# Optimization experiments

Hardware: AMD Instinct MI355X
Metric: run time of the kernel (lower is better)

## Reference

```python
import jax, jax.numpy as jnp
import numpy as np

D_MODEL = 1024
N_HEADS = 16


def setup_inputs() -> dict:
    key = jax.random.key(0)
    k1, k2, k3 = jax.random.split(key, 3)
    B, S = 2, 2048
    std_qkv = (2.0 / (D_MODEL + 3 * D_MODEL)) ** 0.5
    std_out = (2.0 / (D_MODEL + D_MODEL)) ** 0.5
    X = jax.random.normal(k1, (B, S, D_MODEL), dtype=jnp.float32)
    W_qkv = jax.random.normal(k2, (3 * D_MODEL, D_MODEL), dtype=jnp.float32) * std_qkv
    W_out = jax.random.normal(k3, (D_MODEL, D_MODEL), dtype=jnp.float32) * std_out
    return {"X": X, "W_qkv": W_qkv, "W_out": W_out}


def reference(X, W_qkv, W_out):
    B, S, D = X.shape
    H = N_HEADS
    dk = D // H
    # qkv projection: (..., d) @ W^T -> (..., 3d)
    qkv = jnp.einsum('bsd,ed->bse', X, W_qkv)
    Q, K, V = jnp.split(qkv, 3, axis=-1)
    # split heads: (B, S, H*dk) -> (B, H, S, dk)
    def heads(t):
        return t.reshape(B, S, H, dk).transpose(0, 2, 1, 3)
    Q, K, V = heads(Q), heads(K), heads(V)
    # scaled scores (B, H, S, S)
    scores = jnp.einsum('bhqd,bhkd->bhqk', Q, K) / jnp.sqrt(jnp.float32(dk))
    causal = jnp.tril(jnp.ones((S, S), dtype=bool))
    scores = jnp.where(causal, scores.astype(jnp.float32), -jnp.inf)
    weights = jax.nn.softmax(scores, axis=-1).astype(X.dtype)
    out = jnp.einsum('bhqk,bhkd->bhqd', weights, V)
    out = out.transpose(0, 2, 1, 3).reshape(B, S, D)
    return jnp.einsum('bsd,od->bso', out, W_out)
```

## Files before the change

### kernel.cpp

```cpp
#include <hip/hip_runtime.h>

typedef __bf16 bf16;
typedef __bf16 bf16x4v __attribute__((ext_vector_type(4)));
typedef __bf16 bf16x8 __attribute__((ext_vector_type(8)));
typedef float f32x4 __attribute__((ext_vector_type(4)));

#define MFMA16(a, b, c) __builtin_amdgcn_mfma_f32_16x16x32_bf16((a), (b), (c), 0, 0, 0)

#define SEQ 2048
#define DM 1024
#define NH 16

__global__ __launch_bounds__(256) void cvt_bf16(const float* __restrict__ s,
                                                bf16* __restrict__ d, int n4) {
    const int i = blockIdx.x * 256 + threadIdx.x;
    if (i < n4) {
        const float4 v = ((const float4*)s)[i];
        bf16x4v o;
        o.x = (bf16)v.x; o.y = (bf16)v.y; o.z = (bf16)v.z; o.w = (bf16)v.w;
        ((bf16x4v*)d)[i] = o;
    }
}

template <typename CT>
__global__ __launch_bounds__(256) void gemm_nt(const bf16* __restrict__ A,
                                               const bf16* __restrict__ B,
                                               CT* __restrict__ C,
                                               int M, int N, int K) {
    __shared__ bf16 As[128 * 40];
    __shared__ bf16 Bs[128 * 40];

    const int tid = threadIdx.x;
    const int lane = tid & 63, w = tid >> 6;
    const int quad = lane >> 4, l15 = lane & 15;
    const int wm = (w & 1) * 64, wn = (w >> 1) * 64;
    const int rowBase = blockIdx.y * 128, colBase = blockIdx.x * 128;
    const int srow = tid >> 2, sseg = tid & 3;

    f32x4 acc[4][4] = {};

    for (int k0 = 0; k0 < K; k0 += 32) {
        __syncthreads();
#pragma unroll
        for (int r = 0; r < 2; ++r) {
            const int row = srow + r * 64;
            *(bf16x8*)(As + row * 40 + sseg * 8) =
                *(const bf16x8*)(A + (size_t)(rowBase + row) * K + k0 + sseg * 8);
            *(bf16x8*)(Bs + row * 40 + sseg * 8) =
                *(const bf16x8*)(B + (size_t)(colBase + row) * K + k0 + sseg * 8);
        }
        __syncthreads();

        bf16x8 af[4], bfr[4];
#pragma unroll
        for (int i = 0; i < 4; ++i) {
            af[i]  = *(const bf16x8*)(As + (wm + i * 16 + l15) * 40 + quad * 8);
            bfr[i] = *(const bf16x8*)(Bs + (wn + i * 16 + l15) * 40 + quad * 8);
        }
#pragma unroll
        for (int i = 0; i < 4; ++i)
#pragma unroll
            for (int j = 0; j < 4; ++j)
                acc[i][j] = MFMA16(af[i], bfr[j], acc[i][j]);
    }

#pragma unroll
    for (int i = 0; i < 4; ++i)
#pragma unroll
        for (int j = 0; j < 4; ++j)
#pragma unroll
            for (int r = 0; r < 4; ++r)
                C[(size_t)(rowBase + wm + i * 16 + quad * 4 + r) * N +
                  colBase + wn + j * 16 + l15] = (CT)acc[i][j][r];
}

__global__ __launch_bounds__(256) void gemm_qkv(const bf16* __restrict__ A,
                                                const bf16* __restrict__ B,
                                                bf16* __restrict__ qkbuf,
                                                bf16* __restrict__ vtg) {
    __shared__ bf16 As[128 * 40];
    __shared__ bf16 Bs[128 * 40];

    const int K = DM, tid = threadIdx.x;
    const int lane = tid & 63, w = tid >> 6;
    const int quad = lane >> 4, l15 = lane & 15;
    const int wm = (w & 1) * 64, wn = (w >> 1) * 64;
    const int rowBase = blockIdx.y * 128, colBase = blockIdx.x * 128;
    const int srow = tid >> 2, sseg = tid & 3;

    f32x4 acc[4][4] = {};

    for (int k0 = 0; k0 < K; k0 += 32) {
        __syncthreads();
#pragma unroll
        for (int r = 0; r < 2; ++r) {
            const int row = srow + r * 64;
            *(bf16x8*)(As + row * 40 + sseg * 8) =
                *(const bf16x8*)(A + (size_t)(rowBase + row) * K + k0 + sseg * 8);
            *(bf16x8*)(Bs + row * 40 + sseg * 8) =
                *(const bf16x8*)(B + (size_t)(colBase + row) * K + k0 + sseg * 8);
        }
        __syncthreads();

        bf16x8 af[4], bfr[4];
#pragma unroll
        for (int i = 0; i < 4; ++i) {
            af[i]  = *(const bf16x8*)(As + (wm + i * 16 + l15) * 40 + quad * 8);
            bfr[i] = *(const bf16x8*)(Bs + (wn + i * 16 + l15) * 40 + quad * 8);
        }
#pragma unroll
        for (int i = 0; i < 4; ++i)
#pragma unroll
            for (int j = 0; j < 4; ++j)
                acc[i][j] = MFMA16(af[i], bfr[j], acc[i][j]);
    }

    if (colBase < 2 * DM) {
#pragma unroll
        for (int i = 0; i < 4; ++i)
#pragma unroll
            for (int j = 0; j < 4; ++j)
#pragma unroll
                for (int r = 0; r < 4; ++r)
                    qkbuf[(size_t)(rowBase + wm + i * 16 + quad * 4 + r) * 2048 +
                          colBase + wn + j * 16 + l15] = (bf16)acc[i][j][r];
    } else {
#pragma unroll
        for (int i = 0; i < 4; ++i) {
            const int row0 = rowBase + wm + i * 16 + quad * 4;
            const int b = row0 >> 11, s = row0 & 2047;
#pragma unroll
            for (int j = 0; j < 4; ++j) {
                const int col = colBase + wn + j * 16 + l15 - 2 * DM;
                bf16x4v pk;
#pragma unroll
                for (int r = 0; r < 4; ++r) pk[r] = (bf16)acc[i][j][r];
                *(bf16x4v*)(vtg + (size_t)(b * DM + col) * SEQ + s) = pk;
            }
        }
    }
}

__global__ __launch_bounds__(256) void attn_fwd(const bf16* __restrict__ qk,
                                                const bf16* __restrict__ vtg,
                                                bf16* __restrict__ ao) {
    __shared__ bf16 Ks[64 * 72];
    __shared__ bf16 Vts[64 * 72];
    __shared__ bf16 Pt[4][16 * 72];

    const int tid = threadIdx.x;
    const int lane = tid & 63, w = tid >> 6;
    const int quad = lane >> 4, l15 = lane & 15;
    const int bh = blockIdx.x;
    const int qtile = 31 - blockIdx.y;
    const int b = bh >> 4, h = bh & 15;
    const int qbase = qtile * 64;
    const int wq = qbase + w * 16;

    const bf16* qkb = qk + (size_t)b * SEQ * 2048;
    const bf16* vb  = vtg + (size_t)bh * 64 * SEQ;

    bf16x8 q_lo, q_hi;
    {
        const bf16* qp = qkb + (size_t)(wq + l15) * 2048 + h * 64 + quad * 8;
        bf16x8 lo = *(const bf16x8*)qp;
        bf16x8 hi = *(const bf16x8*)(qp + 32);
#pragma unroll
        for (int i = 0; i < 8; ++i) {
            q_lo[i] = (bf16)((float)lo[i] * 0.125f);
            q_hi[i] = (bf16)((float)hi[i] * 0.125f);
        }
    }

    f32x4 o[4] = {};
    float mi = -1e30f, li = 0.f;

    const int kr0 = tid >> 3;
    const int ksg = tid & 7;

    const int nkt = qtile + 1;
    for (int kt = 0; kt < nkt; ++kt) {
        const int k0 = kt * 64;
        __syncthreads();
#pragma unroll
        for (int half = 0; half < 2; ++half) {
            const int kr = kr0 + half * 32;
            *(bf16x8*)(Ks + kr * 72 + ksg * 8) =
                *(const bf16x8*)(qkb + (size_t)(k0 + kr) * 2048 + DM + h * 64 + ksg * 8);
            *(bf16x8*)(Vts + kr * 72 + ksg * 8) =
                *(const bf16x8*)(vb + (size_t)kr * SEQ + k0 + ksg * 8);
        }
        __syncthreads();

        if (k0 <= wq + 15) {
            f32x4 s[4];
#pragma unroll
            for (int t = 0; t < 4; ++t) {
                const bf16* kp = Ks + (t * 16 + l15) * 72 + quad * 8;
                bf16x8 k_lo = *(const bf16x8*)kp;
                bf16x8 k_hi = *(const bf16x8*)(kp + 32);
                f32x4 z = {};
                z = MFMA16(k_lo, q_lo, z);
                z = MFMA16(k_hi, q_hi, z);
                s[t] = z;
            }
            const int qg = wq + l15;
            if (k0 + 63 > wq) {
#pragma unroll
                for (int t = 0; t < 4; ++t)
#pragma unroll
                    for (int r = 0; r < 4; ++r)
                        if (k0 + t * 16 + quad * 4 + r > qg) s[t][r] = -1e30f;
            }
            float mx = s[0][0];
#pragma unroll
            for (int t = 0; t < 4; ++t)
#pragma unroll
                for (int r = 0; r < 4; ++r) mx = fmaxf(mx, s[t][r]);
            mx = fmaxf(mx, __shfl_xor(mx, 16));
            mx = fmaxf(mx, __shfl_xor(mx, 32));
            const float mnew = fmaxf(mi, mx);
            const float alpha = __expf(mi - mnew);
            mi = mnew;

            float rsum = 0.f;
            bf16x4v pb[4];
#pragma unroll
            for (int t = 0; t < 4; ++t)
#pragma unroll
                for (int r = 0; r < 4; ++r) {
                    float p = __expf(s[t][r] - mnew);
                    rsum += p;
                    pb[t][r] = (bf16)p;
                }
            rsum += __shfl_xor(rsum, 16);
            rsum += __shfl_xor(rsum, 32);
            li = li * alpha + rsum;
#pragma unroll
            for (int dt = 0; dt < 4; ++dt)
#pragma unroll
                for (int r = 0; r < 4; ++r) o[dt][r] *= alpha;

            bf16* P = &Pt[w][0];
#pragma unroll
            for (int t = 0; t < 4; ++t)
                *(bf16x4v*)(P + l15 * 72 + t * 16 + quad * 4) = pb[t];
            asm volatile("s_waitcnt lgkmcnt(0)" ::: "memory");

            bf16x8 pf0 = *(const bf16x8*)(P + l15 * 72 + quad * 8);
            bf16x8 pf1 = *(const bf16x8*)(P + l15 * 72 + 32 + quad * 8);
#pragma unroll
            for (int dt = 0; dt < 4; ++dt) {
                const bf16* vp = Vts + (dt * 16 + l15) * 72 + quad * 8;
                bf16x8 v0 = *(const bf16x8*)vp;
                bf16x8 v1 = *(const bf16x8*)(vp + 32);
                o[dt] = MFMA16(v0, pf0, o[dt]);
                o[dt] = MFMA16(v1, pf1, o[dt]);
            }
        }
    }

    const float inv = 1.f / li;
    bf16* aop = ao + (size_t)(b * SEQ + wq + l15) * DM + h * 64;
#pragma unroll
    for (int dt = 0; dt < 4; ++dt) {
        bf16x4v ov;
#pragma unroll
        for (int r = 0; r < 4; ++r) ov[r] = (bf16)(o[dt][r] * inv);
        *(bf16x4v*)(aop + dt * 16 + quad * 4) = ov;
    }
}

extern "C" void kernel_launch(void* const* d_in, const int* in_sizes, int n_in,
                              void* d_out, int out_size, void* d_ws, size_t ws_size,
                              hipStream_t stream) {
    const float* X    = (const float*)d_in[0];
    const float* Wqkv = (const float*)d_in[1];
    const float* Wout = (const float*)d_in[2];
    float* out = (float*)d_out;

    const int M = 2 * SEQ;
    const size_t nX    = (size_t)M * DM;
    const size_t nWqkv = (size_t)3 * DM * DM;
    const size_t nWout = (size_t)DM * DM;
    const size_t nQK   = (size_t)M * 2 * DM;
    const size_t nVT   = (size_t)2 * DM * SEQ;
    const size_t nAO   = (size_t)M * DM;

    if (ws_size < (nX + nWqkv + nWout + nQK + nVT + nAO) * sizeof(bf16)) return;

    bf16* Xb    = (bf16*)d_ws;
    bf16* Wqkvb = Xb + nX;
    bf16* Woutb = Wqkvb + nWqkv;
    bf16* qkbuf = Woutb + nWout;
    bf16* vtg   = qkbuf + nQK;
    bf16* ao    = vtg + nVT;

    cvt_bf16<<<dim3((int)(nX / 4 / 256)),    256, 0, stream>>>(X,    Xb,    (int)(nX / 4));
    cvt_bf16<<<dim3((int)(nWqkv / 4 / 256)), 256, 0, stream>>>(Wqkv, Wqkvb, (int)(nWqkv / 4));
    cvt_bf16<<<dim3((int)(nWout / 4 / 256)), 256, 0, stream>>>(Wout, Woutb, (int)(nWout / 4));

    gemm_qkv<<<dim3(3 * DM / 128, M / 128), 256, 0, stream>>>(Xb, Wqkvb, qkbuf, vtg);
    attn_fwd<<<dim3(2 * NH, SEQ / 64), 256, 0, stream>>>(qkbuf, vtg, ao);
    gemm_nt<float><<<dim3(DM / 128, M / 128), 256, 0, stream>>>(ao, Woutb, out, M, DM, DM);
}
```

Measured before the change: 194.4 us.

## Fuse conversions, stage V transpose via LDS, use 128-key tiles with register prefetch

```diff
diff --git a/kernel.cpp b/kernel.cpp
--- a/kernel.cpp
+++ b/kernel.cpp
@@ -11,15 +11,23 @@
 #define DM 1024
 #define NH 16
 
-__global__ __launch_bounds__(256) void cvt_bf16(const float* __restrict__ s,
-                                                bf16* __restrict__ d, int n4) {
+__global__ __launch_bounds__(256) void cvt_all(const float* __restrict__ X,
+                                               const float* __restrict__ Wq,
+                                               const float* __restrict__ Wo,
+                                               bf16* __restrict__ Xb,
+                                               bf16* __restrict__ Wqb,
+                                               bf16* __restrict__ Wob) {
     const int i = blockIdx.x * 256 + threadIdx.x;
-    if (i < n4) {
-        const float4 v = ((const float4*)s)[i];
-        bf16x4v o;
-        o.x = (bf16)v.x; o.y = (bf16)v.y; o.z = (bf16)v.z; o.w = (bf16)v.w;
-        ((bf16x4v*)d)[i] = o;
-    }
+    const int N1 = (4 * 1024 * 1024) / 4;
+    const int N2 = (3 * 1024 * 1024) / 4;
+    const float* s; bf16* d; int off;
+    if (i < N1)            { s = X;  d = Xb;  off = i; }
+    else if (i < N1 + N2)  { s = Wq; d = Wqb; off = i - N1; }
+    else                   { s = Wo; d = Wob; off = i - N1 - N2; }
+    const float4 v = ((const float4*)s)[off];
+    bf16x4v o;
+    o.x = (bf16)v.x; o.y = (bf16)v.y; o.z = (bf16)v.z; o.w = (bf16)v.w;
+    ((bf16x4v*)d)[off] = o;
 }
 
 template <typename CT>
@@ -78,8 +86,9 @@
                                                 const bf16* __restrict__ B,
                                                 bf16* __restrict__ qkbuf,
                                                 bf16* __restrict__ vtg) {
-    __shared__ bf16 As[128 * 40];
-    __shared__ bf16 Bs[128 * 40];
+    __shared__ bf16 smem[10240];
+    bf16* As = smem;
+    bf16* Bs = smem + 5120;
 
     const int K = DM, tid = threadIdx.x;
     const int lane = tid & 63, w = tid >> 6;
@@ -125,17 +134,32 @@
                     qkbuf[(size_t)(rowBase + wm + i * 16 + quad * 4 + r) * 2048 +
                           colBase + wn + j * 16 + l15] = (bf16)acc[i][j][r];
     } else {
-#pragma unroll
-        for (int i = 0; i < 4; ++i) {
-            const int row0 = rowBase + wm + i * 16 + quad * 4;
-            const int b = row0 >> 11, s = row0 & 2047;
-#pragma unroll
-            for (int j = 0; j < 4; ++j) {
-                const int col = colBase + wn + j * 16 + l15 - 2 * DM;
-                bf16x4v pk;
-#pragma unroll
-                for (int r = 0; r < 4; ++r) pk[r] = (bf16)acc[i][j][r];
-                *(bf16x4v*)(vtg + (size_t)(b * DM + col) * SEQ + s) = pk;
+        bf16* T = smem;
+        const int vcolBase = colBase - 2 * DM;
+        const int bb = rowBase >> 11;
+        const int sBase = rowBase & 2047;
+        const int drow0 = tid >> 4, seg = tid & 15;
+#pragma unroll
+        for (int c = 0; c < 2; ++c) {
+            __syncthreads();
+            if ((w >> 1) == c) {
+#pragma unroll
+                for (int i = 0; i < 4; ++i)
+#pragma unroll
+                    for (int j = 0; j < 4; ++j) {
+                        bf16x4v pk;
+#pragma unroll
+                        for (int r = 0; r < 4; ++r) pk[r] = (bf16)acc[i][j][r];
+                        *(bf16x4v*)(T + (j * 16 + l15) * 136 + wm + i * 16 + quad * 4) = pk;
+                    }
+            }
+            __syncthreads();
+#pragma unroll
+            for (int rr = 0; rr < 4; ++rr) {
+                const int drow = rr * 16 + drow0;
+                *(bf16x8*)(vtg + (size_t)(bb * DM + vcolBase + c * 64 + drow) * SEQ +
+                           sBase + seg * 8) =
+                    *(const bf16x8*)(T + drow * 136 + seg * 8);
             }
         }
     }
@@ -144,9 +168,9 @@
 __global__ __launch_bounds__(256) void attn_fwd(const bf16* __restrict__ qk,
                                                 const bf16* __restrict__ vtg,
                                                 bf16* __restrict__ ao) {
-    __shared__ bf16 Ks[64 * 72];
-    __shared__ bf16 Vts[64 * 72];
-    __shared__ bf16 Pt[4][16 * 72];
+    __shared__ bf16 Ks[128 * 72];
+    __shared__ bf16 Vts[64 * 136];
+    __shared__ bf16 Pt[4][16 * 136];
 
     const int tid = threadIdx.x;
     const int lane = tid & 63, w = tid >> 6;
@@ -175,87 +199,100 @@
     f32x4 o[4] = {};
     float mi = -1e30f, li = 0.f;
 
-    const int kr0 = tid >> 3;
-    const int ksg = tid & 7;
-
-    const int nkt = qtile + 1;
+    bf16x8 pk[4], pv[4];
+    const int nkt = (qbase >> 7) + 1;
+
+    {
+        const int k0 = 0;
+#pragma unroll
+        for (int i = 0; i < 4; ++i) {
+            const int slot = tid + i * 256;
+            pk[i] = *(const bf16x8*)(qkb + (size_t)(k0 + (slot >> 3)) * 2048 + DM + h * 64 + (slot & 7) * 8);
+            pv[i] = *(const bf16x8*)(vb + (size_t)(slot >> 4) * SEQ + k0 + (slot & 15) * 8);
+        }
+    }
+
     for (int kt = 0; kt < nkt; ++kt) {
-        const int k0 = kt * 64;
-        __syncthreads();
-#pragma unroll
-        for (int half = 0; half < 2; ++half) {
-            const int kr = kr0 + half * 32;
-            *(bf16x8*)(Ks + kr * 72 + ksg * 8) =
-                *(const bf16x8*)(qkb + (size_t)(k0 + kr) * 2048 + DM + h * 64 + ksg * 8);
-            *(bf16x8*)(Vts + kr * 72 + ksg * 8) =
-                *(const bf16x8*)(vb + (size_t)kr * SEQ + k0 + ksg * 8);
-        }
-        __syncthreads();
-
-        if (k0 <= wq + 15) {
-            f32x4 s[4];
-#pragma unroll
-            for (int t = 0; t < 4; ++t) {
-                const bf16* kp = Ks + (t * 16 + l15) * 72 + quad * 8;
-                bf16x8 k_lo = *(const bf16x8*)kp;
-                bf16x8 k_hi = *(const bf16x8*)(kp + 32);
-                f32x4 z = {};
-                z = MFMA16(k_lo, q_lo, z);
-                z = MFMA16(k_hi, q_hi, z);
-                s[t] = z;
-            }
-            const int qg = wq + l15;
-            if (k0 + 63 > wq) {
-#pragma unroll
-                for (int t = 0; t < 4; ++t)
-#pragma unroll
-                    for (int r = 0; r < 4; ++r)
-                        if (k0 + t * 16 + quad * 4 + r > qg) s[t][r] = -1e30f;
-            }
-            float mx = s[0][0];
-#pragma unroll
-            for (int t = 0; t < 4; ++t)
-#pragma unroll
-                for (int r = 0; r < 4; ++r) mx = fmaxf(mx, s[t][r]);
-            mx = fmaxf(mx, __shfl_xor(mx, 16));
-            mx = fmaxf(mx, __shfl_xor(mx, 32));
-            const float mnew = fmaxf(mi, mx);
-            const float alpha = __expf(mi - mnew);
-            mi = mnew;
-
-            float rsum = 0.f;
-            bf16x4v pb[4];
-#pragma unroll
-            for (int t = 0; t < 4; ++t)
-#pragma unroll
-                for (int r = 0; r < 4; ++r) {
-                    float p = __expf(s[t][r] - mnew);
-                    rsum += p;
-                    pb[t][r] = (bf16)p;
-                }
-            rsum += __shfl_xor(rsum, 16);
-            rsum += __shfl_xor(rsum, 32);
-            li = li * alpha + rsum;
-#pragma unroll
-            for (int dt = 0; dt < 4; ++dt)
-#pragma unroll
-                for (int r = 0; r < 4; ++r) o[dt][r] *= alpha;
-
-            bf16* P = &Pt[w][0];
-#pragma unroll
-            for (int t = 0; t < 4; ++t)
-                *(bf16x4v*)(P + l15 * 72 + t * 16 + quad * 4) = pb[t];
-            asm volatile("s_waitcnt lgkmcnt(0)" ::: "memory");
-
-            bf16x8 pf0 = *(const bf16x8*)(P + l15 * 72 + quad * 8);
-            bf16x8 pf1 = *(const bf16x8*)(P + l15 * 72 + 32 + quad * 8);
+        const int k0 = kt * 128;
+        __syncthreads();
+#pragma unroll
+        for (int i = 0; i < 4; ++i) {
+            const int slot = tid + i * 256;
+            *(bf16x8*)(Ks + (slot >> 3) * 72 + (slot & 7) * 8) = pk[i];
+            *(bf16x8*)(Vts + (slot >> 4) * 136 + (slot & 15) * 8) = pv[i];
+        }
+        __syncthreads();
+        if (kt + 1 < nkt) {
+            const int kn = k0 + 128;
+#pragma unroll
+            for (int i = 0; i < 4; ++i) {
+                const int slot = tid + i * 256;
+                pk[i] = *(const bf16x8*)(qkb + (size_t)(kn + (slot >> 3)) * 2048 + DM + h * 64 + (slot & 7) * 8);
+                pv[i] = *(const bf16x8*)(vb + (size_t)(slot >> 4) * SEQ + kn + (slot & 15) * 8);
+            }
+        }
+
+        const int t_used = min(8, ((wq + 15 - k0) >> 4) + 1);
+        f32x4 s[8];
+        for (int t = 0; t < t_used; ++t) {
+            const bf16* kp = Ks + (t * 16 + l15) * 72 + quad * 8;
+            bf16x8 k_lo = *(const bf16x8*)kp;
+            bf16x8 k_hi = *(const bf16x8*)(kp + 32);
+            f32x4 z = {};
+            z = MFMA16(k_lo, q_lo, z);
+            z = MFMA16(k_hi, q_hi, z);
+            s[t] = z;
+        }
+        const int qg = wq + l15;
+        if (k0 + 127 > wq) {
+            for (int t = 0; t < t_used; ++t)
+#pragma unroll
+                for (int r = 0; r < 4; ++r)
+                    if (k0 + t * 16 + quad * 4 + r > qg) s[t][r] = -1e30f;
+        }
+        float mx = -1e30f;
+        for (int t = 0; t < t_used; ++t)
+#pragma unroll
+            for (int r = 0; r < 4; ++r) mx = fmaxf(mx, s[t][r]);
+        mx = fmaxf(mx, __shfl_xor(mx, 16));
+        mx = fmaxf(mx, __shfl_xor(mx, 32));
+        const float mnew = fmaxf(mi, mx);
+        const float alpha = __expf(mi - mnew);
+        mi = mnew;
+
+        bf16* P = &Pt[w][0];
+        float rsum = 0.f;
+        for (int t = 0; t < t_used; ++t) {
+            bf16x4v pb;
+#pragma unroll
+            for (int r = 0; r < 4; ++r) {
+                float p = __expf(s[t][r] - mnew);
+                rsum += p;
+                pb[r] = (bf16)p;
+            }
+            *(bf16x4v*)(P + l15 * 136 + t * 16 + quad * 4) = pb;
+        }
+        if (t_used & 1) {
+            bf16x4v z4 = {};
+            *(bf16x4v*)(P + l15 * 136 + t_used * 16 + quad * 4) = z4;
+        }
+        rsum += __shfl_xor(rsum, 16);
+        rsum += __shfl_xor(rsum, 32);
+        li = li * alpha + rsum;
+#pragma unroll
+        for (int dt = 0; dt < 4; ++dt)
+#pragma unroll
+            for (int r = 0; r < 4; ++r) o[dt][r] *= alpha;
+
+        asm volatile("s_waitcnt lgkmcnt(0)" ::: "memory");
+
+        const int f_used = (t_used + 1) >> 1;
+        for (int f = 0; f < f_used; ++f) {
+            bf16x8 pf = *(const bf16x8*)(P + l15 * 136 + f * 32 + quad * 8);
 #pragma unroll
             for (int dt = 0; dt < 4; ++dt) {
-                const bf16* vp = Vts + (dt * 16 + l15) * 72 + quad * 8;
-                bf16x8 v0 = *(const bf16x8*)vp;
-                bf16x8 v1 = *(const bf16x8*)(vp + 32);
-                o[dt] = MFMA16(v0, pf0, o[dt]);
-                o[dt] = MFMA16(v1, pf1, o[dt]);
+                bf16x8 vf = *(const bf16x8*)(Vts + (dt * 16 + l15) * 136 + f * 32 + quad * 8);
+                o[dt] = MFMA16(vf, pf, o[dt]);
             }
         }
     }
@@ -296,9 +333,8 @@
     bf16* vtg   = qkbuf + nQK;
     bf16* ao    = vtg + nVT;
 
-    cvt_bf16<<<dim3((int)(nX / 4 / 256)),    256, 0, stream>>>(X,    Xb,    (int)(nX / 4));
-    cvt_bf16<<<dim3((int)(nWqkv / 4 / 256)), 256, 0, stream>>>(Wqkv, Wqkvb, (int)(nWqkv / 4));
-    cvt_bf16<<<dim3((int)(nWout / 4 / 256)), 256, 0, stream>>>(Wout, Woutb, (int)(nWout / 4));
+    const int nCvt4 = (int)((nX + nWqkv + nWout) / 4);
+    cvt_all<<<dim3(nCvt4 / 256), 256, 0, stream>>>(X, Wqkv, Wout, Xb, Wqkvb, Woutb);
 
     gemm_qkv<<<dim3(3 * DM / 128, M / 128), 256, 0, stream>>>(Xb, Wqkvb, qkbuf, vtg);
     attn_fwd<<<dim3(2 * NH, SEQ / 64), 256, 0, stream>>>(qkbuf, vtg, ao);
```

Measured after the change: 230.3 us. 18.4% more time.

## Fuse conversions, use direct global-to-LDS loads, widen attention q-tiles, retile out GEMM

Applied to the files above, without the earlier changes.

```diff
diff --git a/kernel.cpp b/kernel.cpp
--- a/kernel.cpp
+++ b/kernel.cpp
@@ -11,102 +11,64 @@
 #define DM 1024
 #define NH 16
 
-__global__ __launch_bounds__(256) void cvt_bf16(const float* __restrict__ s,
-                                                bf16* __restrict__ d, int n4) {
+typedef __attribute__((address_space(3))) unsigned int lds_u32;
+typedef __attribute__((address_space(1))) const unsigned int glb_u32;
+
+__device__ __forceinline__ void gld16(const bf16* g, bf16* l) {
+    __builtin_amdgcn_global_load_lds((glb_u32*)g, (lds_u32*)l, 16, 0, 0);
+}
+
+__global__ __launch_bounds__(256) void cvt_all(const float* __restrict__ X,
+                                               const float* __restrict__ Wq,
+                                               const float* __restrict__ Wo,
+                                               bf16* __restrict__ Xb,
+                                               bf16* __restrict__ Wqb,
+                                               bf16* __restrict__ Wob) {
     const int i = blockIdx.x * 256 + threadIdx.x;
-    if (i < n4) {
-        const float4 v = ((const float4*)s)[i];
-        bf16x4v o;
-        o.x = (bf16)v.x; o.y = (bf16)v.y; o.z = (bf16)v.z; o.w = (bf16)v.w;
-        ((bf16x4v*)d)[i] = o;
-    }
-}
-
-template <typename CT>
-__global__ __launch_bounds__(256) void gemm_nt(const bf16* __restrict__ A,
-                                               const bf16* __restrict__ B,
-                                               CT* __restrict__ C,
-                                               int M, int N, int K) {
-    __shared__ bf16 As[128 * 40];
-    __shared__ bf16 Bs[128 * 40];
-
-    const int tid = threadIdx.x;
-    const int lane = tid & 63, w = tid >> 6;
-    const int quad = lane >> 4, l15 = lane & 15;
-    const int wm = (w & 1) * 64, wn = (w >> 1) * 64;
-    const int rowBase = blockIdx.y * 128, colBase = blockIdx.x * 128;
-    const int srow = tid >> 2, sseg = tid & 3;
-
-    f32x4 acc[4][4] = {};
-
-    for (int k0 = 0; k0 < K; k0 += 32) {
-        __syncthreads();
-#pragma unroll
-        for (int r = 0; r < 2; ++r) {
-            const int row = srow + r * 64;
-            *(bf16x8*)(As + row * 40 + sseg * 8) =
-                *(const bf16x8*)(A + (size_t)(rowBase + row) * K + k0 + sseg * 8);
-            *(bf16x8*)(Bs + row * 40 + sseg * 8) =
-                *(const bf16x8*)(B + (size_t)(colBase + row) * K + k0 + sseg * 8);
-        }
-        __syncthreads();
-
-        bf16x8 af[4], bfr[4];
-#pragma unroll
-        for (int i = 0; i < 4; ++i) {
-            af[i]  = *(const bf16x8*)(As + (wm + i * 16 + l15) * 40 + quad * 8);
-            bfr[i] = *(const bf16x8*)(Bs + (wn + i * 16 + l15) * 40 + quad * 8);
-        }
-#pragma unroll
-        for (int i = 0; i < 4; ++i)
-#pragma unroll
-            for (int j = 0; j < 4; ++j)
-                acc[i][j] = MFMA16(af[i], bfr[j], acc[i][j]);
-    }
-
-#pragma unroll
-    for (int i = 0; i < 4; ++i)
-#pragma unroll
-        for (int j = 0; j < 4; ++j)
-#pragma unroll
-            for (int r = 0; r < 4; ++r)
-                C[(size_t)(rowBase + wm + i * 16 + quad * 4 + r) * N +
-                  colBase + wn + j * 16 + l15] = (CT)acc[i][j][r];
+    const int N1 = (4 * 1024 * 1024) / 4;
+    const int N2 = (3 * 1024 * 1024) / 4;
+    const float* s; bf16* d; int off;
+    if (i < N1)            { s = X;  d = Xb;  off = i; }
+    else if (i < N1 + N2)  { s = Wq; d = Wqb; off = i - N1; }
+    else                   { s = Wo; d = Wob; off = i - N1 - N2; }
+    const float4 v = ((const float4*)s)[off];
+    bf16x4v o;
+    o.x = (bf16)v.x; o.y = (bf16)v.y; o.z = (bf16)v.z; o.w = (bf16)v.w;
+    ((bf16x4v*)d)[off] = o;
 }
 
 __global__ __launch_bounds__(256) void gemm_qkv(const bf16* __restrict__ A,
                                                 const bf16* __restrict__ B,
                                                 bf16* __restrict__ qkbuf,
                                                 bf16* __restrict__ vtg) {
-    __shared__ bf16 As[128 * 40];
-    __shared__ bf16 Bs[128 * 40];
+    __shared__ bf16 As[128 * 32];
+    __shared__ bf16 Bs[128 * 32];
 
     const int K = DM, tid = threadIdx.x;
     const int lane = tid & 63, w = tid >> 6;
     const int quad = lane >> 4, l15 = lane & 15;
     const int wm = (w & 1) * 64, wn = (w >> 1) * 64;
     const int rowBase = blockIdx.y * 128, colBase = blockIdx.x * 128;
-    const int srow = tid >> 2, sseg = tid & 3;
 
     f32x4 acc[4][4] = {};
 
     for (int k0 = 0; k0 < K; k0 += 32) {
         __syncthreads();
 #pragma unroll
-        for (int r = 0; r < 2; ++r) {
-            const int row = srow + r * 64;
-            *(bf16x8*)(As + row * 40 + sseg * 8) =
-                *(const bf16x8*)(A + (size_t)(rowBase + row) * K + k0 + sseg * 8);
-            *(bf16x8*)(Bs + row * 40 + sseg * 8) =
-                *(const bf16x8*)(B + (size_t)(colBase + row) * K + k0 + sseg * 8);
+        for (int i = 0; i < 2; ++i) {
+            const int c = w * 64 + i * 256 + lane;
+            gld16(A + (size_t)(rowBase + (c >> 2)) * K + k0 + (c & 3) * 8,
+                  As + (w * 64 + i * 256) * 8);
+            gld16(B + (size_t)(colBase + (c >> 2)) * K + k0 + (c & 3) * 8,
+                  Bs + (w * 64 + i * 256) * 8);
         }
         __syncthreads();
 
         bf16x8 af[4], bfr[4];
 #pragma unroll
         for (int i = 0; i < 4; ++i) {
-            af[i]  = *(const bf16x8*)(As + (wm + i * 16 + l15) * 40 + quad * 8);
-            bfr[i] = *(const bf16x8*)(Bs + (wn + i * 16 + l15) * 40 + quad * 8);
+            af[i]  = *(const bf16x8*)(As + (wm + i * 16 + l15) * 32 + quad * 8);
+            bfr[i] = *(const bf16x8*)(Bs + (wn + i * 16 + l15) * 32 + quad * 8);
         }
 #pragma unroll
         for (int i = 0; i < 4; ++i)
@@ -128,17 +90,70 @@
 #pragma unroll
         for (int i = 0; i < 4; ++i) {
             const int row0 = rowBase + wm + i * 16 + quad * 4;
-            const int b = row0 >> 11, s = row0 & 2047;
+            const int bb = row0 >> 11, s = row0 & 2047;
 #pragma unroll
             for (int j = 0; j < 4; ++j) {
                 const int col = colBase + wn + j * 16 + l15 - 2 * DM;
                 bf16x4v pk;
 #pragma unroll
                 for (int r = 0; r < 4; ++r) pk[r] = (bf16)acc[i][j][r];
-                *(bf16x4v*)(vtg + (size_t)(b * DM + col) * SEQ + s) = pk;
-            }
-        }
-    }
+                *(bf16x4v*)(vtg + (size_t)(bb * DM + col) * SEQ + s) = pk;
+            }
+        }
+    }
+}
+
+__global__ __launch_bounds__(256) void gemm_out(const bf16* __restrict__ A,
+                                                const bf16* __restrict__ B,
+                                                float* __restrict__ C) {
+    __shared__ bf16 As[64 * 32];
+    __shared__ bf16 Bs[128 * 32];
+
+    const int K = DM, N = DM, tid = threadIdx.x;
+    const int lane = tid & 63, w = tid >> 6;
+    const int quad = lane >> 4, l15 = lane & 15;
+    const int wm = (w & 1) * 32, wn = (w >> 1) * 64;
+    const int rowBase = blockIdx.y * 64, colBase = blockIdx.x * 128;
+
+    f32x4 acc[2][4] = {};
+
+    for (int k0 = 0; k0 < K; k0 += 32) {
+        __syncthreads();
+        {
+            const int c = w * 64 + lane;
+            gld16(A + (size_t)(rowBase + (c >> 2)) * K + k0 + (c & 3) * 8,
+                  As + (w * 64) * 8);
+        }
+#pragma unroll
+        for (int i = 0; i < 2; ++i) {
+            const int c = w * 64 + i * 256 + lane;
+            gld16(B + (size_t)(colBase + (c >> 2)) * K + k0 + (c & 3) * 8,
+                  Bs + (w * 64 + i * 256) * 8);
+        }
+        __syncthreads();
+
+        bf16x8 af[2], bfr[4];
+#pragma unroll
+        for (int i = 0; i < 2; ++i)
+            af[i]  = *(const bf16x8*)(As + (wm + i * 16 + l15) * 32 + quad * 8);
+#pragma unroll
+        for (int j = 0; j < 4; ++j)
+            bfr[j] = *(const bf16x8*)(Bs + (wn + j * 16 + l15) * 32 + quad * 8);
+#pragma unroll
+        for (int i = 0; i < 2; ++i)
+#pragma unroll
+            for (int j = 0; j < 4; ++j)
+                acc[i][j] = MFMA16(af[i], bfr[j], acc[i][j]);
+    }
+
+#pragma unroll
+    for (int i = 0; i < 2; ++i)
+#pragma unroll
+        for (int j = 0; j < 4; ++j)
+#pragma unroll
+            for (int r = 0; r < 4; ++r)
+                C[(size_t)(rowBase + wm + i * 16 + quad * 4 + r) * N +
+                  colBase + wn + j * 16 + l15] = acc[i][j][r];
 }
 
 __global__ __launch_bounds__(256) void attn_fwd(const bf16* __restrict__ qk,
@@ -152,33 +167,37 @@
     const int lane = tid & 63, w = tid >> 6;
     const int quad = lane >> 4, l15 = lane & 15;
     const int bh = blockIdx.x;
-    const int qtile = 31 - blockIdx.y;
+    const int qt = 15 - blockIdx.y;
     const int b = bh >> 4, h = bh & 15;
-    const int qbase = qtile * 64;
-    const int wq = qbase + w * 16;
+    const int qbase = qt * 128;
+    const int g0 = qbase + w * 16;
+    const int g1 = qbase + 64 + w * 16;
 
     const bf16* qkb = qk + (size_t)b * SEQ * 2048;
     const bf16* vb  = vtg + (size_t)bh * 64 * SEQ;
 
-    bf16x8 q_lo, q_hi;
+    bf16x8 q0lo, q0hi, q1lo, q1hi;
     {
-        const bf16* qp = qkb + (size_t)(wq + l15) * 2048 + h * 64 + quad * 8;
-        bf16x8 lo = *(const bf16x8*)qp;
-        bf16x8 hi = *(const bf16x8*)(qp + 32);
+        const bf16* qp0 = qkb + (size_t)(g0 + l15) * 2048 + h * 64 + quad * 8;
+        const bf16* qp1 = qkb + (size_t)(g1 + l15) * 2048 + h * 64 + quad * 8;
+        bf16x8 a0 = *(const bf16x8*)qp0, b0 = *(const bf16x8*)(qp0 + 32);
+        bf16x8 a1 = *(const bf16x8*)qp1, b1 = *(const bf16x8*)(qp1 + 32);
 #pragma unroll
         for (int i = 0; i < 8; ++i) {
-            q_lo[i] = (bf16)((float)lo[i] * 0.125f);
-            q_hi[i] = (bf16)((float)hi[i] * 0.125f);
-        }
-    }
-
-    f32x4 o[4] = {};
-    float mi = -1e30f, li = 0.f;
+            q0lo[i] = (bf16)((float)a0[i] * 0.125f);
+            q0hi[i] = (bf16)((float)b0[i] * 0.125f);
+            q1lo[i] = (bf16)((float)a1[i] * 0.125f);
+            q1hi[i] = (bf16)((float)b1[i] * 0.125f);
+        }
+    }
+
+    f32x4 o0[4] = {}, o1[4] = {};
+    float m0 = -1e30f, l0 = 0.f, m1 = -1e30f, l1 = 0.f;
 
     const int kr0 = tid >> 3;
     const int ksg = tid & 7;
 
-    const int nkt = qtile + 1;
+    const int nkt = (qbase >> 6) + 2;
     for (int kt = 0; kt < nkt; ++kt) {
         const int k0 = kt * 64;
         __syncthreads();
@@ -192,20 +211,21 @@
         }
         __syncthreads();
 
-        if (k0 <= wq + 15) {
+        auto process = [&](const bf16x8& qlo, const bf16x8& qhi, int g,
+                           float& mi, float& li, f32x4* o) {
             f32x4 s[4];
 #pragma unroll
             for (int t = 0; t < 4; ++t) {
                 const bf16* kp = Ks + (t * 16 + l15) * 72 + quad * 8;
-                bf16x8 k_lo = *(const bf16x8*)kp;
-                bf16x8 k_hi = *(const bf16x8*)(kp + 32);
+                bf16x8 klo = *(const bf16x8*)kp;
+                bf16x8 khi = *(const bf16x8*)(kp + 32);
                 f32x4 z = {};
-                z = MFMA16(k_lo, q_lo, z);
-                z = MFMA16(k_hi, q_hi, z);
+                z = MFMA16(klo, qlo, z);
+                z = MFMA16(khi, qhi, z);
                 s[t] = z;
             }
-            const int qg = wq + l15;
-            if (k0 + 63 > wq) {
+            const int qg = g + l15;
+            if (k0 + 63 > g) {
 #pragma unroll
                 for (int t = 0; t < 4; ++t)
 #pragma unroll
@@ -224,15 +244,18 @@
             mi = mnew;
 
             float rsum = 0.f;
-            bf16x4v pb[4];
-#pragma unroll
-            for (int t = 0; t < 4; ++t)
+            bf16* P = &Pt[w][0];
+#pragma unroll
+            for (int t = 0; t < 4; ++t) {
+                bf16x4v pb;
 #pragma unroll
                 for (int r = 0; r < 4; ++r) {
                     float p = __expf(s[t][r] - mnew);
                     rsum += p;
-                    pb[t][r] = (bf16)p;
+                    pb[r] = (bf16)p;
                 }
+                *(bf16x4v*)(P + l15 * 72 + t * 16 + quad * 4) = pb;
+            }
             rsum += __shfl_xor(rsum, 16);
             rsum += __shfl_xor(rsum, 32);
             li = li * alpha + rsum;
@@ -241,12 +264,7 @@
 #pragma unroll
                 for (int r = 0; r < 4; ++r) o[dt][r] *= alpha;
 
-            bf16* P = &Pt[w][0];
-#pragma unroll
-            for (int t = 0; t < 4; ++t)
-                *(bf16x4v*)(P + l15 * 72 + t * 16 + quad * 4) = pb[t];
             asm volatile("s_waitcnt lgkmcnt(0)" ::: "memory");
-
             bf16x8 pf0 = *(const bf16x8*)(P + l15 * 72 + quad * 8);
             bf16x8 pf1 = *(const bf16x8*)(P + l15 * 72 + 32 + quad * 8);
 #pragma unroll
@@ -257,17 +275,25 @@
                 o[dt] = MFMA16(v0, pf0, o[dt]);
                 o[dt] = MFMA16(v1, pf1, o[dt]);
             }
-        }
-    }
-
-    const float inv = 1.f / li;
-    bf16* aop = ao + (size_t)(b * SEQ + wq + l15) * DM + h * 64;
+        };
+
+        process(q1lo, q1hi, g1, m1, l1, o1);
+        if (k0 <= g0 + 15) process(q0lo, q0hi, g0, m0, l0, o0);
+    }
+
+    const float i0 = 1.f / l0, i1 = 1.f / l1;
+    bf16* a0 = ao + (size_t)(b * SEQ + g0 + l15) * DM + h * 64;
+    bf16* a1 = ao + (size_t)(b * SEQ + g1 + l15) * DM + h * 64;
 #pragma unroll
     for (int dt = 0; dt < 4; ++dt) {
-        bf16x4v ov;
-#pragma unroll
-        for (int r = 0; r < 4; ++r) ov[r] = (bf16)(o[dt][r] * inv);
-        *(bf16x4v*)(aop + dt * 16 + quad * 4) = ov;
+        bf16x4v v0, v1;
+#pragma unroll
+        for (int r = 0; r < 4; ++r) {
+            v0[r] = (bf16)(o0[dt][r] * i0);
+            v1[r] = (bf16)(o1[dt][r] * i1);
+        }
+        *(bf16x4v*)(a0 + dt * 16 + quad * 4) = v0;
+        *(bf16x4v*)(a1 + dt * 16 + quad * 4) = v1;
     }
 }
 
@@ -296,11 +322,10 @@
     bf16* vtg   = qkbuf + nQK;
     bf16* ao    = vtg + nVT;
 
-    cvt_bf16<<<dim3((int)(nX / 4 / 256)),    256, 0, stream>>>(X,    Xb,    (int)(nX / 4));
-    cvt_bf16<<<dim3((int)(nWqkv / 4 / 256)), 256, 0, stream>>>(Wqkv, Wqkvb, (int)(nWqkv / 4));
-    cvt_bf16<<<dim3((int)(nWout / 4 / 256)), 256, 0, stream>>>(Wout, Woutb, (int)(nWout / 4));
+    const int nCvt4 = (int)((nX + nWqkv + nWout) / 4);
+    cvt_all<<<dim3(nCvt4 / 256), 256, 0, stream>>>(X, Wqkv, Wout, Xb, Wqkvb, Woutb);
 
     gemm_qkv<<<dim3(3 * DM / 128, M / 128), 256, 0, stream>>>(Xb, Wqkvb, qkbuf, vtg);
-    attn_fwd<<<dim3(2 * NH, SEQ / 64), 256, 0, stream>>>(qkbuf, vtg, ao);
-    gemm_nt<float><<<dim3(DM / 128, M / 128), 256, 0, stream>>>(ao, Woutb, out, M, DM, DM);
-}
+    attn_fwd<<<dim3(2 * NH, SEQ / 128), 256, 0, stream>>>(qkbuf, vtg, ao);
+    gemm_out<<<dim3(DM / 128, M / 64), 256, 0, stream>>>(ao, Woutb, out);
+}
```

Result: slower. 200.6 us (+3.2%).
